# Kernel optimization log

Measured on AMD Instinct MI355X. Metric: run time of the kernel, lower is better.

## Reference

```python
import jax, jax.numpy as jnp
import numpy as np

N = 4096        # batch nodes
E = 65536       # random edges (self-loops appended -> 69632 total)
F_IN = 256
H = 128
C = 2
MIN = 1024      # minority (class 1) count; first MIN nodes
REP = 2         # int(N_pct/100) synthetic reps per minority sample


def setup_inputs() -> dict:
    key = jax.random.key(0)
    ks = jax.random.split(key, 24)
    feat = jax.random.normal(ks[0], (N, F_IN), dtype=jnp.float32)
    src = jax.random.randint(ks[1], (E,), 0, N, dtype=jnp.int32)
    dst = jax.random.randint(ks[2], (E,), 0, N, dtype=jnp.int32)
    loops = jnp.arange(N, dtype=jnp.int32)
    src = jnp.concatenate([src, loops])
    dst = jnp.concatenate([dst, loops])
    # dense batch adjacency (target for EdgeLoss), A[i,j]=1 if edge j->i
    adj = jnp.zeros((N, N), dtype=jnp.float32).at[dst, src].set(1.0)
    # deterministic labels: first MIN nodes are minority class 1
    labels = jnp.concatenate([jnp.ones((MIN,), jnp.int32), jnp.zeros((N - MIN,), jnp.int32)])

    def w(k, shape, fan_in):
        return jax.random.normal(k, shape, dtype=jnp.float32) / np.sqrt(fan_in)

    params = dict(
        W_pool0=w(ks[3], (F_IN, F_IN), F_IN), b_pool0=jnp.zeros((F_IN,), jnp.float32),
        W_self0=w(ks[4], (H, F_IN), F_IN), W_neigh0=w(ks[5], (H, F_IN), F_IN), b0=jnp.zeros((H,), jnp.float32),
        W_pool1=w(ks[6], (H, H), H), b_pool1=jnp.zeros((H,), jnp.float32),
        W_self1=w(ks[7], (H, H), H), W_neigh1=w(ks[8], (H, H), H), b1=jnp.zeros((H,), jnp.float32),
        de_weight=jax.random.uniform(ks[9], (H, H), jnp.float32, -1.0 / np.sqrt(H), 1.0 / np.sqrt(H)),
        W_conv=w(ks[10], (H, 2 * H), 2 * H),
        W_clf=w(ks[11], (C, H), H), b_clf=jnp.zeros((C,), jnp.float32),
        gaps=jax.random.uniform(ks[12], (MIN, REP), jnp.float32),  # SMOTE interpolation gaps
    )
    return dict(feat=feat, adj=adj, src=src, dst=dst, labels=labels, **params)


def _sage_pool_layer(h, src, dst, W_pool, b_pool, W_self, W_neigh, b):
    # DGL SAGEConv aggregator_type='pool': max over neighbors of relu(fc_pool(h))
    p = jax.nn.relu(h @ W_pool.T + b_pool)                     # [N, d]
    hn = jax.ops.segment_max(p[src], dst, num_segments=h.shape[0])
    hn = jnp.where(jnp.isfinite(hn), hn, 0.0)
    return h @ W_self.T + hn @ W_neigh.T + b


def _l2norm(x, eps=1e-12):
    return x / jnp.maximum(jnp.linalg.norm(x, axis=1, keepdims=True), eps)


def _smote_nn_interp(cand, gaps):
    # pairwise euclidean distances (vectorized form of the per-row loop)
    sq = jnp.sum(cand * cand, axis=1)
    d2 = sq[:, None] + sq[None, :] - 2.0 * (cand @ cand.T)
    dist = jnp.sqrt(jnp.maximum(d2, 0.0))
    nn_idx = jnp.argsort(dist, axis=1)[:, 1]                   # k=2 -> single nearest (excl. self)
    diff = cand[nn_idx] - cand                                  # [MIN, H]
    synth = cand[:, None, :] + gaps[:, :, None] * diff[:, None, :]  # [MIN, REP, H], i-major order
    return synth.reshape(MIN * REP, cand.shape[1])


def reference(feat, adj, src, dst, labels,
              W_pool0, b_pool0, W_self0, W_neigh0, b0,
              W_pool1, b_pool1, W_self1, W_neigh1, b1,
              de_weight, W_conv, W_clf, b_clf, gaps):
    # ---- Encoder (2 SAGEConv 'pool' layers; dropout is eval-mode identity) ----
    h = _sage_pool_layer(feat, src, dst, W_pool0, b_pool0, W_self0, W_neigh0, b0)
    h = _l2norm(jax.nn.relu(h))
    h = _sage_pool_layer(h, src, dst, W_pool1, b_pool1, W_self1, W_neigh1, b1)
    # ---- SMOTE (minority = first MIN rows, by deterministic label construction) ----
    synth = _smote_nn_interp(h[:MIN], gaps)
    x = jnp.concatenate([h, synth], axis=0)                    # [N + MIN*REP, H]
    y = jnp.concatenate([labels, jnp.ones((MIN * REP,), jnp.int32)])
    # ---- Decoder: sigmoid(out @ out.T) ----
    out = x @ de_weight.T
    pred_adj = jax.nn.sigmoid(out @ out.T)                     # [6144, 6144]
    # ---- EdgeLoss vs dense batch adjacency ----
    rec = pred_adj[:N, :N]
    edge_num = jnp.sum(adj != 0).astype(jnp.float32)
    neg_w = edge_num / (float(N * N) - edge_num)
    weight = jnp.where(adj == 0, neg_w, 1.0)
    loss = jnp.sum(weight * (rec - adj) ** 2)
    # ---- threshold + SageClassifier (1 layer, no activation before clf) ----
    pred_adj = jnp.where(pred_adj >= 0.5, pred_adj, 0.0)
    neigh = (pred_adj @ x) / (jnp.sum(pred_adj, axis=1, keepdims=True) + 1.0)
    hc = jnp.concatenate([x, neigh], axis=-1) @ W_conv.T
    logits = hc @ W_clf.T + b_clf                              # [6144, 2]
    return logits, y, loss
```

## Files before the change

### kernel.cpp

```cpp
#include <hip/hip_runtime.h>
#include <cstddef>

typedef unsigned short ushort_t;
typedef __attribute__((ext_vector_type(8))) short bf16x8;
typedef __attribute__((ext_vector_type(4))) float f32x4;
typedef __attribute__((ext_vector_type(16))) float f32x16;

#define WS_P0     0u
#define WS_DOTS   0u
#define WS_OBK    524288u
#define WS_HN0    1048576u
#define WS_HC     1048576u
#define WS_H1     2097152u
#define WS_H1N    2621440u
#define WS_P1     3145728u
#define WS_PVB    3145728u
#define WS_HN1    3670016u
#define WS_H2     4194304u
#define WS_X      4718592u
#define WS_BITMAP 5767168u
#define WS_NEIGH  6291456u
#define WS_ROWSUM 7077888u
#define WS_SCAL   7084032u
#define WS_DEG    7084048u
#define WS_NN     7088144u
#define WS_CUR    7089168u
#define WS_ROWPTR 7093264u
#define WS_EIDX   7097361u

__device__ inline ushort_t f2bf(float f) {
  unsigned u = __float_as_uint(f);
  u += 0x7fff + ((u >> 16) & 1);
  return (ushort_t)(u >> 16);
}

__global__ __launch_bounds__(256, 2) void gemm_nt(
    const float* __restrict__ A, int lda,
    const float* __restrict__ B, int ldb,
    const float* __restrict__ A2, int lda2,
    const float* __restrict__ B2, int ldb2,
    const float* __restrict__ bias,
    float* __restrict__ C, int ldc,
    int K, int relu,
    ushort_t* __restrict__ Cb,
    const float* __restrict__ a2scale,
    const float* __restrict__ Ahi)
{
  __shared__ float As[16][68];
  __shared__ float Bs[16][68];
  const int tid = threadIdx.x;
  const int tx = tid & 15, ty = tid >> 4;
  const int lr = tid >> 2;
  const int lk = (tid & 3) << 2;
  const int i0 = blockIdx.y << 6;
  const int j0 = blockIdx.x << 6;
  float acc[4][4] = {};
  const int npass = (A2 != nullptr) ? 2 : 1;
  for (int pass = 0; pass < npass; ++pass) {
    const float* Ap = pass ? A2 : A; const int la = pass ? lda2 : lda;
    const float* Bp = pass ? B2 : B; const int lb = pass ? ldb2 : ldb;
    const float sc = (pass && a2scale) ? __frcp_rn(a2scale[i0 + lr] + 1.f) : 1.f;
    const float* Arow = (pass == 0 && Ahi != nullptr && i0 >= 4096)
        ? (Ahi + (size_t)(i0 - 4096 + lr) * la)
        : (Ap + (size_t)(i0 + lr) * la);
    for (int k0 = 0; k0 < K; k0 += 16) {
      float4 ag = *(const float4*)(Arow + (k0 + lk));
      const float4 bg = *(const float4*)(Bp + (size_t)(j0 + lr) * lb + (k0 + lk));
      ag.x *= sc; ag.y *= sc; ag.z *= sc; ag.w *= sc;
      __syncthreads();
      As[lk+0][lr]=ag.x; As[lk+1][lr]=ag.y; As[lk+2][lr]=ag.z; As[lk+3][lr]=ag.w;
      Bs[lk+0][lr]=bg.x; Bs[lk+1][lr]=bg.y; Bs[lk+2][lr]=bg.z; Bs[lk+3][lr]=bg.w;
      __syncthreads();
#pragma unroll
      for (int k = 0; k < 16; ++k) {
        const float4 a4 = *(const float4*)&As[k][ty << 2];
        const float4 b4 = *(const float4*)&Bs[k][tx << 2];
        const float aa[4] = {a4.x, a4.y, a4.z, a4.w};
        const float bb[4] = {b4.x, b4.y, b4.z, b4.w};
#pragma unroll
        for (int ii = 0; ii < 4; ++ii)
#pragma unroll
          for (int jj = 0; jj < 4; ++jj)
            acc[ii][jj] += aa[ii] * bb[jj];
      }
    }
  }
  float badd[4] = {0.f, 0.f, 0.f, 0.f};
  if (bias) {
    const float4 t = *(const float4*)(bias + j0 + (tx << 2));
    badd[0]=t.x; badd[1]=t.y; badd[2]=t.z; badd[3]=t.w;
  }
#pragma unroll
  for (int ii = 0; ii < 4; ++ii) {
    float4 o;
    o.x = acc[ii][0] + badd[0];
    o.y = acc[ii][1] + badd[1];
    o.z = acc[ii][2] + badd[2];
    o.w = acc[ii][3] + badd[3];
    if (relu) { o.x=fmaxf(o.x,0.f); o.y=fmaxf(o.y,0.f); o.z=fmaxf(o.z,0.f); o.w=fmaxf(o.w,0.f); }
    if (Cb) {
      const int i_ = i0 + (ty << 2) + ii;
      const int j_ = j0 + (tx << 2);
      const size_t off = ((size_t)(i_ >> 5) << 12) +
                         (size_t)(((j_ >> 4) << 9) +
                                  ((((( j_ >> 3) & 1) << 5) + (i_ & 31)) << 3) +
                                  (j_ & 7));
      ushort4 ob4;
      ob4.x = f2bf(o.x); ob4.y = f2bf(o.y); ob4.z = f2bf(o.z); ob4.w = f2bf(o.w);
      *(ushort4*)(Cb + off) = ob4;
    } else {
      const size_t off = (size_t)(i0 + (ty<<2) + ii) * ldc + j0 + (tx<<2);
      *(float4*)(C + off) = o;
    }
  }
}

__global__ void count_bitmap_k(const int* __restrict__ src, const int* __restrict__ dst,
                               int* __restrict__ deg, unsigned* __restrict__ bitmap, int E) {
  const int e = blockIdx.x * 256 + threadIdx.x;
  if (e < E) {
    const int d_ = dst[e], s_ = src[e];
    atomicAdd(&deg[d_], 1);
    const unsigned cell = ((unsigned)d_ << 12) + (unsigned)s_;
    atomicOr(&bitmap[cell >> 5], 1u << (cell & 31));
  }
}

__global__ __launch_bounds__(1024) void scan_k(const int* __restrict__ deg,
                                               int* __restrict__ rowptr,
                                               int* __restrict__ cursor) {
  __shared__ int sums[1024];
  const int t = threadIdx.x;
  const int4 d = *(const int4*)(deg + (t << 2));
  const int local = d.x + d.y + d.z + d.w;
  sums[t] = local;
  __syncthreads();
  for (int off = 1; off < 1024; off <<= 1) {
    int v = (t >= off) ? sums[t - off] : 0;
    __syncthreads();
    sums[t] += v;
    __syncthreads();
  }
  const int excl = sums[t] - local;
  const int o0 = excl, o1 = o0 + d.x, o2 = o1 + d.y, o3 = o2 + d.z;
  rowptr[(t<<2)+0]=o0; rowptr[(t<<2)+1]=o1; rowptr[(t<<2)+2]=o2; rowptr[(t<<2)+3]=o3;
  cursor[(t<<2)+0]=o0; cursor[(t<<2)+1]=o1; cursor[(t<<2)+2]=o2; cursor[(t<<2)+3]=o3;
  if (t == 1023) rowptr[4096] = sums[1023];
}

__global__ void fill_k(const int* __restrict__ src, const int* __restrict__ dst,
                       int* __restrict__ cursor, int* __restrict__ eidx, int E) {
  const int e = blockIdx.x * 256 + threadIdx.x;
  if (e < E) {
    const int p = atomicAdd(&cursor[dst[e]], 1);
    eidx[p] = src[e];
  }
}

__global__ void segmax_k(const float* __restrict__ p, const int* __restrict__ rowptr,
                         const int* __restrict__ eidx, float* __restrict__ hn, int F) {
  const int row = blockIdx.x, f = threadIdx.x;
  const int b = rowptr[row], e = rowptr[row + 1];
  float m = 0.f;
  for (int k = b; k < e; ++k) m = fmaxf(m, p[(size_t)eidx[k] * F + f]);
  hn[(size_t)row * F + f] = m;
}

__device__ inline float wave_sum(float v) {
#pragma unroll
  for (int o = 32; o > 0; o >>= 1) v += __shfl_down(v, o, 64);
  return v;
}

__global__ void relu_l2norm_k(const float* __restrict__ in, float* __restrict__ out) {
  const int row = blockIdx.x, f = threadIdx.x;
  const float v = fmaxf(in[(size_t)row * 128 + f], 0.f);
  const float ss = wave_sum(v * v);
  __shared__ float w[2];
  if ((f & 63) == 0) w[f >> 6] = ss;
  __syncthreads();
  const float denom = fmaxf(sqrtf(w[0] + w[1]), 1e-12f);
  out[(size_t)row * 128 + f] = v / denom;
}

__global__ void argmin_k(const float* __restrict__ dots, int* __restrict__ nn) {
  __shared__ float sqd[1024];
  const int i = blockIdx.x, tid = threadIdx.x;
#pragma unroll
  for (int z = 0; z < 4; ++z) {
    const int j = (tid << 2) + z;
    sqd[j] = dots[(size_t)j * 1025];
  }
  __syncthreads();
  float best = 3.402823466e38f; int bidx = 0x7fffffff;
  const float si = sqd[i];
  for (int j = tid; j < 1024; j += 256) {
    if (j == i) continue;
    float d2 = si + sqd[j] - 2.f * dots[(size_t)i * 1024 + j];
    d2 = fmaxf(d2, 0.f);
    if (d2 < best || (d2 == best && j < bidx)) { best = d2; bidx = j; }
  }
  __shared__ float bv[256]; __shared__ int bi[256];
  bv[tid] = best; bi[tid] = bidx;
  __syncthreads();
  for (int s = 128; s > 0; s >>= 1) {
    if (tid < s) {
      if (bv[tid+s] < bv[tid] || (bv[tid+s] == bv[tid] && bi[tid+s] < bi[tid])) {
        bv[tid] = bv[tid+s]; bi[tid] = bi[tid+s];
      }
    }
    __syncthreads();
  }
  if (tid == 0) nn[i] = bi[0];
}

__global__ __launch_bounds__(256) void build_pack_k(
    const float* __restrict__ h2, const int* __restrict__ nn,
    const float* __restrict__ gaps, float* __restrict__ synth,
    ushort_t* __restrict__ pvb) {
  __shared__ ushort_t s[4096];
  const int jt = blockIdx.x, tid = threadIdx.x;
  if (jt < 128) {
    const float* ip = h2 + ((size_t)jt << 12);
#pragma unroll
    for (int k = 0; k < 4; ++k) {
      const float4 v = *(const float4*)(ip + (tid << 4) + (k << 2));
      ushort4 h; h.x = f2bf(v.x); h.y = f2bf(v.y); h.z = f2bf(v.z); h.w = f2bf(v.w);
      *(ushort4*)(s + (tid << 4) + (k << 2)) = h;
    }
  } else {
    const int row = tid >> 3;
    const int sIdx = ((jt - 128) << 5) + row;
    const int i = sIdx >> 1;
    const float g = gaps[sIdx];
    const int ni = nn[i];
#pragma unroll
    for (int k = 0; k < 4; ++k) {
      const int f = ((tid & 7) << 4) + (k << 2);
      const float4 c4 = *(const float4*)(h2 + (size_t)i * 128 + f);
      const float4 n4 = *(const float4*)(h2 + (size_t)ni * 128 + f);
      float4 v;
      v.x = c4.x + g * (n4.x - c4.x);
      v.y = c4.y + g * (n4.y - c4.y);
      v.z = c4.z + g * (n4.z - c4.z);
      v.w = c4.w + g * (n4.w - c4.w);
      *(float4*)(synth + (size_t)sIdx * 128 + f) = v;
      ushort4 h; h.x = f2bf(v.x); h.y = f2bf(v.y); h.z = f2bf(v.z); h.w = f2bf(v.w);
      *(ushort4*)(s + (row << 7) + f) = h;
    }
  }
  __syncthreads();
  const int u = tid & 31, ft = (tid >> 5) & 3, cc = tid >> 7;
  ushort_t* op = pvb + ((size_t)jt << 12) + (cc << 11) + (ft << 9);
#pragma unroll
  for (int m = 0; m < 2; ++m) {
    const int l = (u << 1) + m;
    const int f = (ft << 5) + (l & 31);
    const int jb = (cc << 4) + ((l >> 5) << 3);
    ushort4 o0, o1;
    o0.x = s[(jb + 0) * 128 + f]; o0.y = s[(jb + 1) * 128 + f];
    o0.z = s[(jb + 2) * 128 + f]; o0.w = s[(jb + 3) * 128 + f];
    o1.x = s[(jb + 4) * 128 + f]; o1.y = s[(jb + 5) * 128 + f];
    o1.z = s[(jb + 6) * 128 + f]; o1.w = s[(jb + 7) * 128 + f];
    *(ushort4*)(op + (l << 3) + 0) = o0;
    *(ushort4*)(op + (l << 3) + 4) = o1;
  }
}

__global__ __launch_bounds__(256, 2) void fused_mfma(
    const ushort_t* __restrict__ obk,
    const ushort_t* __restrict__ pvb,
    const unsigned* __restrict__ bitmap,
    float* __restrict__ neigh,
    float* __restrict__ rowsum,
    float* __restrict__ scal)
{
  __shared__ float wred[4][4];
  const int tid = threadIdx.x;
  const int w = tid >> 6;
  const int lane = tid & 63;
  const int lo = lane & 31, hi = lane >> 5;
  const int it = (blockIdx.x << 2) + w;
  const int iw = it << 5;
  const int jt0 = blockIdx.y << 4;
  const bool loss_i = (it < 128);

  bf16x8 qf[8];
  {
    const ushort_t* qp = obk + ((size_t)it << 12) + (lane << 3);
#pragma unroll
    for (int c = 0; c < 8; ++c) qf[c] = *(const bf16x8*)(qp + (c << 9));
  }
  f32x16 oacc[4];
#pragma unroll
  for (int ft = 0; ft < 4; ++ft)
#pragma unroll
    for (int r = 0; r < 16; ++r) oacc[ft][r] = 0.f;
  float rs = 0.f, s_all = 0.f, s1a = 0.f, suba = 0.f, ecf = 0.f;

  bf16x8 a[8];
  {
    const ushort_t* kp = obk + ((size_t)jt0 << 12) + (lane << 3);
#pragma unroll
    for (int c = 0; c < 8; ++c) a[c] = *(const bf16x8*)(kp + (c << 9));
  }
  f32x16 sp;
#pragma unroll
  for (int r = 0; r < 16; ++r) sp[r] = 0.f;
#pragma unroll
  for (int c = 0; c < 8; ++c)
    sp = __builtin_amdgcn_mfma_f32_32x32x16_bf16(a[c], qf[c], sp, 0, 0, 0);
  {
    const ushort_t* kp = obk + ((size_t)(jt0 + 1) << 12) + (lane << 3);
#pragma unroll
    for (int c = 0; c < 8; ++c) a[c] = *(const bf16x8*)(kp + (c << 9));
  }

  for (int t = 0; t < 16; ++t) {
    const int jt = jt0 + t;
    bf16x8 bvf[2][4];
    {
      const ushort_t* vp = pvb + ((size_t)jt << 12) + (lane << 3);
#pragma unroll
      for (int cc = 0; cc < 2; ++cc)
#pragma unroll
        for (int ft = 0; ft < 4; ++ft)
          bvf[cc][ft] = *(const bf16x8*)(vp + (cc << 11) + (ft << 9));
    }
    f32x16 sn;
#pragma unroll
    for (int r = 0; r < 16; ++r) sn[r] = 0.f;
    if (t < 15) {
#pragma unroll
      for (int c = 0; c < 8; ++c)
        sn = __builtin_amdgcn_mfma_f32_32x32x16_bf16(a[c], qf[c], sn, 0, 0, 0);
    }
    if (t < 14) {
      const ushort_t* kp = obk + ((size_t)(jt + 2) << 12) + (lane << 3);
#pragma unroll
      for (int c = 0; c < 8; ++c) a[c] = *(const bf16x8*)(kp + (c << 9));
    }
    const bool loss_t = loss_i && (jt < 128);
    unsigned word = 0u;
    if (loss_t) word = bitmap[((unsigned)(iw + lo) << 7) + (unsigned)jt];
    float p[16];
    if (loss_t) {
      ecf += (float)__popc(word & (0x0F0F0F0Fu << (hi << 2)));
#pragma unroll
      for (int r = 0; r < 16; ++r) {
        const float v = sp[r];
        const float sg = __builtin_amdgcn_rcpf(1.f + __expf(-v));
        const int jl = (r & 3) + ((r >> 2) << 3) + (hi << 2);
        const float e_ = (float)((word >> jl) & 1u);
        s_all += sg * sg;
        s1a  += e_ * (sg - 1.f) * (sg - 1.f);
        suba += e_ * sg * sg;
        const float tv = (v >= 0.f) ? sg : 0.f;
        p[r] = tv; rs += tv;
      }
    } else {
#pragma unroll
      for (int r = 0; r < 16; ++r) {
        const float v = sp[r];
        const float sg = __builtin_amdgcn_rcpf(1.f + __expf(-v));
        const float tv = (v >= 0.f) ? sg : 0.f;
        p[r] = tv; rs += tv;
      }
    }
#pragma unroll
    for (int cc = 0; cc < 2; ++cc) {
      const int b8 = cc << 3;
      unsigned c01, c23, c45, c67;
      asm("v_cvt_pk_bf16_f32 %0, %1, %2" : "=v"(c01) : "v"(p[b8+0]), "v"(p[b8+1]));
      asm("v_cvt_pk_bf16_f32 %0, %1, %2" : "=v"(c23) : "v"(p[b8+2]), "v"(p[b8+3]));
      asm("v_cvt_pk_bf16_f32 %0, %1, %2" : "=v"(c45) : "v"(p[b8+4]), "v"(p[b8+5]));
      asm("v_cvt_pk_bf16_f32 %0, %1, %2" : "=v"(c67) : "v"(p[b8+6]), "v"(p[b8+7]));
      const auto w0 = __builtin_amdgcn_permlane32_swap((int)c01, (int)c45, false, false);
      const auto w1 = __builtin_amdgcn_permlane32_swap((int)c23, (int)c67, false, false);
      union { int i[4]; bf16x8 h; } u;
      u.i[0] = w0[0]; u.i[1] = w1[0]; u.i[2] = w0[1]; u.i[3] = w1[1];
#pragma unroll
      for (int ft = 0; ft < 4; ++ft)
        oacc[ft] = __builtin_amdgcn_mfma_f32_32x32x16_bf16(u.h, bvf[cc][ft], oacc[ft], 0, 0, 0);
    }
    sp = sn;
  }
#pragma unroll
  for (int ft = 0; ft < 4; ++ft)
#pragma unroll
    for (int r = 0; r < 16; ++r) {
      const int ir = (r & 3) + ((r >> 2) << 3) + (hi << 2);
      atomicAdd(&neigh[(size_t)(iw + ir) * 128 + (ft << 5) + lo], oacc[ft][r]);
    }
  rs += __shfl_xor(rs, 32, 64);
  if (hi == 0) atomicAdd(&rowsum[iw + lo], rs);
  {
    float v0 = wave_sum(s_all), v1 = wave_sum(s1a), v2 = wave_sum(suba), v3 = wave_sum(ecf);
    if (lane == 0) { wred[w][0] = v0; wred[w][1] = v1; wred[w][2] = v2; wred[w][3] = v3; }
  }
  __syncthreads();
  if (tid < 4) {
    const float t = wred[0][tid] + wred[1][tid] + wred[2][tid] + wred[3][tid];
    const int dst = (tid == 0) ? 0 : (tid == 1) ? 1 : (tid == 2) ? 3 : 4;
    atomicAdd(&scal[dst], t);
  }
}

__global__ void logits_y_loss_k(const float* __restrict__ hc, const float* __restrict__ Wclf,
                                const float* __restrict__ bclf, const int* __restrict__ labels,
                                const float* __restrict__ scal,
                                float* __restrict__ outp) {
  const int i = blockIdx.x, f = threadIdx.x;
  const float h = hc[(size_t)i * 128 + f];
  const float v0 = wave_sum(h * Wclf[f]);
  const float v1 = wave_sum(h * Wclf[128 + f]);
  __shared__ float w0[2], w1[2];
  if ((f & 63) == 0) { w0[f >> 6] = v0; w1[f >> 6] = v1; }
  __syncthreads();
  if (f == 0) {
    outp[(size_t)i * 2 + 0] = w0[0] + w0[1] + bclf[0];
    outp[(size_t)i * 2 + 1] = w1[0] + w1[1] + bclf[1];
    outp[12288 + i] = (i < 4096) ? (float)labels[i] : 1.f;
    if (i == 0) {
      const float cnt = scal[4];
      const float neg_w = cnt / (16777216.f - cnt);
      outp[18432] = neg_w * (scal[0] - scal[3]) + scal[1];
    }
  }
}

extern "C" void kernel_launch(void* const* d_in, const int* in_sizes, int n_in,
                              void* d_out, int out_size, void* d_ws, size_t ws_size,
                              hipStream_t stream) {
  const float* feat     = (const float*)d_in[0];
  const int*   src      = (const int*)d_in[2];
  const int*   dst      = (const int*)d_in[3];
  const int*   labels   = (const int*)d_in[4];
  const float* W_pool0  = (const float*)d_in[5];
  const float* b_pool0  = (const float*)d_in[6];
  const float* W_self0  = (const float*)d_in[7];
  const float* W_neigh0 = (const float*)d_in[8];
  const float* b0       = (const float*)d_in[9];
  const float* W_pool1  = (const float*)d_in[10];
  const float* b_pool1  = (const float*)d_in[11];
  const float* W_self1  = (const float*)d_in[12];
  const float* W_neigh1 = (const float*)d_in[13];
  const float* b1       = (const float*)d_in[14];
  const float* de_w     = (const float*)d_in[15];
  const float* W_conv   = (const float*)d_in[16];
  const float* W_clf    = (const float*)d_in[17];
  const float* b_clf    = (const float*)d_in[18];
  const float* gaps     = (const float*)d_in[19];
  const int E = in_sizes[2];

  float* ws = (float*)d_ws;
  float* p0       = ws + WS_P0;
  float* dots     = ws + WS_DOTS;
  ushort_t* obk   = (ushort_t*)(ws + WS_OBK);
  float* hn0      = ws + WS_HN0;
  unsigned* bitmap= (unsigned*)(ws + WS_BITMAP);
  float* hc       = ws + WS_HC;
  float* h1       = ws + WS_H1;
  float* h1n      = ws + WS_H1N;
  float* p1       = ws + WS_P1;
  ushort_t* pvb   = (ushort_t*)(ws + WS_PVB);
  float* hn1      = ws + WS_HN1;
  float* h2       = ws + WS_H2;
  float* synth    = ws + WS_X;
  float* neigh    = ws + WS_NEIGH;
  float* rowsum   = ws + WS_ROWSUM;
  float* scal     = ws + WS_SCAL;
  int* deg        = (int*)(ws + WS_DEG);
  int* nn         = (int*)(ws + WS_NN);
  int* cursor     = (int*)(ws + WS_CUR);
  int* rowptr     = (int*)(ws + WS_ROWPTR);
  int* eidx       = (int*)(ws + WS_EIDX);

  float* outp = (float*)d_out;
  const dim3 blk(256);

  hipMemsetAsync(bitmap, 0, (size_t)(WS_DEG + 4096 - WS_BITMAP) * 4, stream);

  count_bitmap_k<<<(E + 255) / 256, blk, 0, stream>>>(src, dst, deg, bitmap, E);
  scan_k<<<1, 1024, 0, stream>>>(deg, rowptr, cursor);
  fill_k<<<(E + 255) / 256, blk, 0, stream>>>(src, dst, cursor, eidx, E);

  gemm_nt<<<dim3(4, 64), blk, 0, stream>>>(feat, 256, W_pool0, 256,
                                           nullptr, 0, nullptr, 0,
                                           b_pool0, p0, 256, 256, 1, nullptr, nullptr, nullptr);
  segmax_k<<<4096, 256, 0, stream>>>(p0, rowptr, eidx, hn0, 256);
  gemm_nt<<<dim3(2, 64), blk, 0, stream>>>(feat, 256, W_self0, 256,
                                           hn0, 256, W_neigh0, 256,
                                           b0, h1, 128, 256, 0, nullptr, nullptr, nullptr);
  relu_l2norm_k<<<4096, 128, 0, stream>>>(h1, h1n);

  gemm_nt<<<dim3(2, 64), blk, 0, stream>>>(h1n, 128, W_pool1, 128,
                                           nullptr, 0, nullptr, 0,
                                           b_pool1, p1, 128, 128, 1, nullptr, nullptr, nullptr);
  segmax_k<<<4096, 128, 0, stream>>>(p1, rowptr, eidx, hn1, 128);
  gemm_nt<<<dim3(2, 64), blk, 0, stream>>>(h1n, 128, W_self1, 128,
                                           hn1, 128, W_neigh1, 128,
                                           b1, h2, 128, 128, 0, nullptr, nullptr, nullptr);

  gemm_nt<<<dim3(16, 16), blk, 0, stream>>>(h2, 128, h2, 128,
                                            nullptr, 0, nullptr, 0,
                                            nullptr, dots, 1024, 128, 0, nullptr, nullptr, nullptr);
  argmin_k<<<1024, 256, 0, stream>>>(dots, nn);
  build_pack_k<<<192, blk, 0, stream>>>(h2, nn, gaps, synth, pvb);

  gemm_nt<<<dim3(2, 96), blk, 0, stream>>>(h2, 128, de_w, 128,
                                           nullptr, 0, nullptr, 0,
                                           nullptr, nullptr, 0, 128, 0, obk, nullptr, synth);
  fused_mfma<<<dim3(48, 12), blk, 0, stream>>>(obk, pvb, bitmap, neigh, rowsum, scal);

  gemm_nt<<<dim3(2, 96), blk, 0, stream>>>(h2, 128, W_conv, 256,
                                           neigh, 128, W_conv + 128, 256,
                                           nullptr, hc, 128, 128, 0, nullptr, rowsum, synth);
  logits_y_loss_k<<<6144, 128, 0, stream>>>(hc, W_clf, b_clf, labels, scal, outp);

  (void)n_in; (void)out_size; (void)ws_size; (void)in_sizes;
}
```

Measured before the change: 357.2 us.

## Replace FP32 SIMT GEMM with split-bf16 MFMA GEMM and simplify score pipelining

The generic small GEMM now runs on MFMA matrix cores. Each fp32 operand is split into a high and a low bf16 part, and three MFMA products are used to approximate fp32 accuracy. The fused decoder kernel drops its one-tile-ahead score software pipeline. It now computes the current tile's scores in two independent accumulators and prefetches only the next key tile. This trades explicit MFMA/ALU overlap for shorter dependency chains and fewer live registers, with small precision differences in the GEMMs.

```diff
diff --git a/kernel.cpp b/kernel.cpp
--- a/kernel.cpp
+++ b/kernel.cpp
@@ -33,8 +33,11 @@
   u += 0x7fff + ((u >> 16) & 1);
   return (ushort_t)(u >> 16);
 }
-
-__global__ __launch_bounds__(256, 2) void gemm_nt(
+__device__ inline float bf2f(ushort_t h) {
+  return __uint_as_float((unsigned)h << 16);
+}
+
+__global__ __launch_bounds__(256, 2) void mgemm(
     const float* __restrict__ A, int lda,
     const float* __restrict__ B, int ldb,
     const float* __restrict__ A2, int lda2,
@@ -46,71 +49,81 @@
     const float* __restrict__ a2scale,
     const float* __restrict__ Ahi)
 {
-  __shared__ float As[16][68];
-  __shared__ float Bs[16][68];
+  __shared__ ushort_t AhS[64][36], AlS[64][36], BhS[64][36], BlS[64][36];
   const int tid = threadIdx.x;
-  const int tx = tid & 15, ty = tid >> 4;
+  const int lane = tid & 63;
+  const int w = tid >> 6;
+  const int lo = lane & 31, hi = lane >> 5;
+  const int iq = (w & 1) << 5, jq = (w >> 1) << 5;
+  const int i0 = blockIdx.y << 6, j0 = blockIdx.x << 6;
   const int lr = tid >> 2;
-  const int lk = (tid & 3) << 2;
-  const int i0 = blockIdx.y << 6;
-  const int j0 = blockIdx.x << 6;
-  float acc[4][4] = {};
+  const int c8 = (tid & 3) << 3;
+  f32x16 acc;
+#pragma unroll
+  for (int t = 0; t < 16; ++t) acc[t] = 0.f;
   const int npass = (A2 != nullptr) ? 2 : 1;
   for (int pass = 0; pass < npass; ++pass) {
     const float* Ap = pass ? A2 : A; const int la = pass ? lda2 : lda;
     const float* Bp = pass ? B2 : B; const int lb = pass ? ldb2 : ldb;
+    const float* Arow = (pass == 0 && Ahi != nullptr && (i0 + lr) >= 4096)
+        ? (Ahi + (size_t)(i0 + lr - 4096) * la)
+        : (Ap + (size_t)(i0 + lr) * la);
+    const float* Brow = Bp + (size_t)(j0 + lr) * lb;
     const float sc = (pass && a2scale) ? __frcp_rn(a2scale[i0 + lr] + 1.f) : 1.f;
-    const float* Arow = (pass == 0 && Ahi != nullptr && i0 >= 4096)
-        ? (Ahi + (size_t)(i0 - 4096 + lr) * la)
-        : (Ap + (size_t)(i0 + lr) * la);
-    for (int k0 = 0; k0 < K; k0 += 16) {
-      float4 ag = *(const float4*)(Arow + (k0 + lk));
-      const float4 bg = *(const float4*)(Bp + (size_t)(j0 + lr) * lb + (k0 + lk));
-      ag.x *= sc; ag.y *= sc; ag.z *= sc; ag.w *= sc;
+    for (int k0 = 0; k0 < K; k0 += 32) {
+      float av[8], bv[8];
+      {
+        const float4 a0 = *(const float4*)(Arow + k0 + c8);
+        const float4 a1 = *(const float4*)(Arow + k0 + c8 + 4);
+        const float4 b0 = *(const float4*)(Brow + k0 + c8);
+        const float4 b1 = *(const float4*)(Brow + k0 + c8 + 4);
+        av[0]=a0.x*sc; av[1]=a0.y*sc; av[2]=a0.z*sc; av[3]=a0.w*sc;
+        av[4]=a1.x*sc; av[5]=a1.y*sc; av[6]=a1.z*sc; av[7]=a1.w*sc;
+        bv[0]=b0.x; bv[1]=b0.y; bv[2]=b0.z; bv[3]=b0.w;
+        bv[4]=b1.x; bv[5]=b1.y; bv[6]=b1.z; bv[7]=b1.w;
+      }
       __syncthreads();
-      As[lk+0][lr]=ag.x; As[lk+1][lr]=ag.y; As[lk+2][lr]=ag.z; As[lk+3][lr]=ag.w;
-      Bs[lk+0][lr]=bg.x; Bs[lk+1][lr]=bg.y; Bs[lk+2][lr]=bg.z; Bs[lk+3][lr]=bg.w;
+      {
+        ushort_t ah8[8], al8[8], bh8[8], bl8[8];
+#pragma unroll
+        for (int e = 0; e < 8; ++e) {
+          const ushort_t ah = f2bf(av[e]);
+          ah8[e] = ah; al8[e] = f2bf(av[e] - bf2f(ah));
+          const ushort_t bh = f2bf(bv[e]);
+          bh8[e] = bh; bl8[e] = f2bf(bv[e] - bf2f(bh));
+        }
+        *(bf16x8*)&AhS[lr][c8] = *(bf16x8*)ah8;
+        *(bf16x8*)&AlS[lr][c8] = *(bf16x8*)al8;
+        *(bf16x8*)&BhS[lr][c8] = *(bf16x8*)bh8;
+        *(bf16x8*)&BlS[lr][c8] = *(bf16x8*)bl8;
+      }
       __syncthreads();
 #pragma unroll
-      for (int k = 0; k < 16; ++k) {
-        const float4 a4 = *(const float4*)&As[k][ty << 2];
-        const float4 b4 = *(const float4*)&Bs[k][tx << 2];
-        const float aa[4] = {a4.x, a4.y, a4.z, a4.w};
-        const float bb[4] = {b4.x, b4.y, b4.z, b4.w};
-#pragma unroll
-        for (int ii = 0; ii < 4; ++ii)
-#pragma unroll
-          for (int jj = 0; jj < 4; ++jj)
-            acc[ii][jj] += aa[ii] * bb[jj];
+      for (int kk = 0; kk < 32; kk += 16) {
+        const bf16x8 ahf = *(const bf16x8*)&AhS[iq + lo][kk + (hi << 3)];
+        const bf16x8 alf = *(const bf16x8*)&AlS[iq + lo][kk + (hi << 3)];
+        const bf16x8 bhf = *(const bf16x8*)&BhS[jq + lo][kk + (hi << 3)];
+        const bf16x8 blf = *(const bf16x8*)&BlS[jq + lo][kk + (hi << 3)];
+        acc = __builtin_amdgcn_mfma_f32_32x32x16_bf16(ahf, bhf, acc, 0, 0, 0);
+        acc = __builtin_amdgcn_mfma_f32_32x32x16_bf16(alf, bhf, acc, 0, 0, 0);
+        acc = __builtin_amdgcn_mfma_f32_32x32x16_bf16(ahf, blf, acc, 0, 0, 0);
       }
     }
   }
-  float badd[4] = {0.f, 0.f, 0.f, 0.f};
-  if (bias) {
-    const float4 t = *(const float4*)(bias + j0 + (tx << 2));
-    badd[0]=t.x; badd[1]=t.y; badd[2]=t.z; badd[3]=t.w;
-  }
-#pragma unroll
-  for (int ii = 0; ii < 4; ++ii) {
-    float4 o;
-    o.x = acc[ii][0] + badd[0];
-    o.y = acc[ii][1] + badd[1];
-    o.z = acc[ii][2] + badd[2];
-    o.w = acc[ii][3] + badd[3];
-    if (relu) { o.x=fmaxf(o.x,0.f); o.y=fmaxf(o.y,0.f); o.z=fmaxf(o.z,0.f); o.w=fmaxf(o.w,0.f); }
+  const int col = j0 + jq + lo;
+  const float badd = bias ? bias[col] : 0.f;
+#pragma unroll
+  for (int t = 0; t < 16; ++t) {
+    float o = acc[t] + badd;
+    if (relu) o = fmaxf(o, 0.f);
+    const int row = i0 + iq + (t & 3) + ((t >> 2) << 3) + (hi << 2);
     if (Cb) {
-      const int i_ = i0 + (ty << 2) + ii;
-      const int j_ = j0 + (tx << 2);
-      const size_t off = ((size_t)(i_ >> 5) << 12) +
-                         (size_t)(((j_ >> 4) << 9) +
-                                  ((((( j_ >> 3) & 1) << 5) + (i_ & 31)) << 3) +
-                                  (j_ & 7));
-      ushort4 ob4;
-      ob4.x = f2bf(o.x); ob4.y = f2bf(o.y); ob4.z = f2bf(o.z); ob4.w = f2bf(o.w);
-      *(ushort4*)(Cb + off) = ob4;
+      const size_t off = ((size_t)(row >> 5) << 12) +
+          (size_t)(((col >> 4) << 9) +
+                   (((((col >> 3) & 1) << 5) + (row & 31)) << 3) + (col & 7));
+      Cb[off] = f2bf(o);
     } else {
-      const size_t off = (size_t)(i0 + (ty<<2) + ii) * ldc + j0 + (tx<<2);
-      *(float4*)(C + off) = o;
+      C[(size_t)row * ldc + col] = o;
     }
   }
 }
@@ -304,20 +317,17 @@
 #pragma unroll
     for (int c = 0; c < 8; ++c) a[c] = *(const bf16x8*)(kp + (c << 9));
   }
-  f32x16 sp;
-#pragma unroll
-  for (int r = 0; r < 16; ++r) sp[r] = 0.f;
-#pragma unroll
-  for (int c = 0; c < 8; ++c)
-    sp = __builtin_amdgcn_mfma_f32_32x32x16_bf16(a[c], qf[c], sp, 0, 0, 0);
-  {
-    const ushort_t* kp = obk + ((size_t)(jt0 + 1) << 12) + (lane << 3);
-#pragma unroll
-    for (int c = 0; c < 8; ++c) a[c] = *(const bf16x8*)(kp + (c << 9));
-  }
 
   for (int t = 0; t < 16; ++t) {
     const int jt = jt0 + t;
+    f32x16 s0, s1;
+#pragma unroll
+    for (int r = 0; r < 16; ++r) { s0[r] = 0.f; s1[r] = 0.f; }
+#pragma unroll
+    for (int c = 0; c < 4; ++c) {
+      s0 = __builtin_amdgcn_mfma_f32_32x32x16_bf16(a[c], qf[c], s0, 0, 0, 0);
+      s1 = __builtin_amdgcn_mfma_f32_32x32x16_bf16(a[c + 4], qf[c + 4], s1, 0, 0, 0);
+    }
     bf16x8 bvf[2][4];
     {
       const ushort_t* vp = pvb + ((size_t)jt << 12) + (lane << 3);
@@ -327,16 +337,8 @@
         for (int ft = 0; ft < 4; ++ft)
           bvf[cc][ft] = *(const bf16x8*)(vp + (cc << 11) + (ft << 9));
     }
-    f32x16 sn;
-#pragma unroll
-    for (int r = 0; r < 16; ++r) sn[r] = 0.f;
     if (t < 15) {
-#pragma unroll
-      for (int c = 0; c < 8; ++c)
-        sn = __builtin_amdgcn_mfma_f32_32x32x16_bf16(a[c], qf[c], sn, 0, 0, 0);
-    }
-    if (t < 14) {
-      const ushort_t* kp = obk + ((size_t)(jt + 2) << 12) + (lane << 3);
+      const ushort_t* kp = obk + ((size_t)(jt + 1) << 12) + (lane << 3);
 #pragma unroll
       for (int c = 0; c < 8; ++c) a[c] = *(const bf16x8*)(kp + (c << 9));
     }
@@ -348,7 +350,7 @@
       ecf += (float)__popc(word & (0x0F0F0F0Fu << (hi << 2)));
 #pragma unroll
       for (int r = 0; r < 16; ++r) {
-        const float v = sp[r];
+        const float v = s0[r] + s1[r];
         const float sg = __builtin_amdgcn_rcpf(1.f + __expf(-v));
         const int jl = (r & 3) + ((r >> 2) << 3) + (hi << 2);
         const float e_ = (float)((word >> jl) & 1u);
@@ -361,7 +363,7 @@
     } else {
 #pragma unroll
       for (int r = 0; r < 16; ++r) {
-        const float v = sp[r];
+        const float v = s0[r] + s1[r];
         const float sg = __builtin_amdgcn_rcpf(1.f + __expf(-v));
         const float tv = (v >= 0.f) ? sg : 0.f;
         p[r] = tv; rs += tv;
@@ -383,7 +385,6 @@
       for (int ft = 0; ft < 4; ++ft)
         oacc[ft] = __builtin_amdgcn_mfma_f32_32x32x16_bf16(u.h, bvf[cc][ft], oacc[ft], 0, 0, 0);
     }
-    sp = sn;
   }
 #pragma unroll
   for (int ft = 0; ft < 4; ++ft)
@@ -458,8 +459,8 @@
   float* dots     = ws + WS_DOTS;
   ushort_t* obk   = (ushort_t*)(ws + WS_OBK);
   float* hn0      = ws + WS_HN0;
+  float* hc       = ws + WS_HC;
   unsigned* bitmap= (unsigned*)(ws + WS_BITMAP);
-  float* hc       = ws + WS_HC;
   float* h1       = ws + WS_H1;
   float* h1n      = ws + WS_H1N;
   float* p1       = ws + WS_P1;
@@ -485,37 +486,37 @@
   scan_k<<<1, 1024, 0, stream>>>(deg, rowptr, cursor);
   fill_k<<<(E + 255) / 256, blk, 0, stream>>>(src, dst, cursor, eidx, E);
 
-  gemm_nt<<<dim3(4, 64), blk, 0, stream>>>(feat, 256, W_pool0, 256,
-                                           nullptr, 0, nullptr, 0,
-                                           b_pool0, p0, 256, 256, 1, nullptr, nullptr, nullptr);
+  mgemm<<<dim3(4, 64), blk, 0, stream>>>(feat, 256, W_pool0, 256,
+                                         nullptr, 0, nullptr, 0,
+                                         b_pool0, p0, 256, 256, 1, nullptr, nullptr, nullptr);
   segmax_k<<<4096, 256, 0, stream>>>(p0, rowptr, eidx, hn0, 256);
-  gemm_nt<<<dim3(2, 64), blk, 0, stream>>>(feat, 256, W_self0, 256,
-                                           hn0, 256, W_neigh0, 256,
-                                           b0, h1, 128, 256, 0, nullptr, nullptr, nullptr);
+  mgemm<<<dim3(2, 64), blk, 0, stream>>>(feat, 256, W_self0, 256,
+                                         hn0, 256, W_neigh0, 256,
+                                         b0, h1, 128, 256, 0, nullptr, nullptr, nullptr);
   relu_l2norm_k<<<4096, 128, 0, stream>>>(h1, h1n);
 
-  gemm_nt<<<dim3(2, 64), blk, 0, stream>>>(h1n, 128, W_pool1, 128,
-                                           nullptr, 0, nullptr, 0,
-                                           b_pool1, p1, 128, 128, 1, nullptr, nullptr, nullptr);
+  mgemm<<<dim3(2, 64), blk, 0, stream>>>(h1n, 128, W_pool1, 128,
+                                         nullptr, 0, nullptr, 0,
+                                         b_pool1, p1, 128, 128, 1, nullptr, nullptr, nullptr);
   segmax_k<<<4096, 128, 0, stream>>>(p1, rowptr, eidx, hn1, 128);
-  gemm_nt<<<dim3(2, 64), blk, 0, stream>>>(h1n, 128, W_self1, 128,
-                                           hn1, 128, W_neigh1, 128,
-                                           b1, h2, 128, 128, 0, nullptr, nullptr, nullptr);
-
-  gemm_nt<<<dim3(16, 16), blk, 0, stream>>>(h2, 128, h2, 128,
-                                            nullptr, 0, nullptr, 0,
-                                            nullptr, dots, 1024, 128, 0, nullptr, nullptr, nullptr);
+  mgemm<<<dim3(2, 64), blk, 0, stream>>>(h1n, 128, W_self1, 128,
+                                         hn1, 128, W_neigh1, 128,
+                                         b1, h2, 128, 128, 0, nullptr, nullptr, nullptr);
+
+  mgemm<<<dim3(16, 16), blk, 0, stream>>>(h2, 128, h2, 128,
+                                          nullptr, 0, nullptr, 0,
+                                          nullptr, dots, 1024, 128, 0, nullptr, nullptr, nullptr);
   argmin_k<<<1024, 256, 0, stream>>>(dots, nn);
   build_pack_k<<<192, blk, 0, stream>>>(h2, nn, gaps, synth, pvb);
 
-  gemm_nt<<<dim3(2, 96), blk, 0, stream>>>(h2, 128, de_w, 128,
-                                           nullptr, 0, nullptr, 0,
-                                           nullptr, nullptr, 0, 128, 0, obk, nullptr, synth);
+  mgemm<<<dim3(2, 96), blk, 0, stream>>>(h2, 128, de_w, 128,
+                                         nullptr, 0, nullptr, 0,
+                                         nullptr, nullptr, 0, 128, 0, obk, nullptr, synth);
   fused_mfma<<<dim3(48, 12), blk, 0, stream>>>(obk, pvb, bitmap, neigh, rowsum, scal);
 
-  gemm_nt<<<dim3(2, 96), blk, 0, stream>>>(h2, 128, W_conv, 256,
-                                           neigh, 128, W_conv + 128, 256,
-                                           nullptr, hc, 128, 128, 0, nullptr, rowsum, synth);
+  mgemm<<<dim3(2, 96), blk, 0, stream>>>(h2, 128, W_conv, 256,
+                                         neigh, 128, W_conv + 128, 256,
+                                         nullptr, hc, 128, 128, 0, nullptr, rowsum, synth);
   logits_y_loss_k<<<6144, 128, 0, stream>>>(hc, W_clf, b_clf, labels, scal, outp);
 
   (void)n_in; (void)out_size; (void)ws_size; (void)in_sizes;
```

Result: faster. 312.0 us (-12.7%).
